# Performance work log

Hardware: AMD Instinct MI355X
Metric: run time of the kernel (lower is better)

Reference implementation:

```python
import jax, jax.numpy as jnp
import numpy as np

EPS = 1e-8
LRELU_SLOPE = 0.2
ACT_GAIN = float(np.sqrt(2.0))  # def_gain for lrelu
GAIN = 1.0                      # forward default
CLAMP = 256.0


def setup_inputs() -> dict:
    key = jax.random.key(0)
    k1, k2 = jax.random.split(key)
    x = jax.random.normal(k1, (8, 128, 32, 32, 32), dtype=jnp.float32)
    weight = jax.random.normal(k2, (128, 128, 3, 3, 3), dtype=jnp.float32)
    bias = jnp.zeros((128,), dtype=jnp.float32)
    return {"x": x, "weight": weight, "bias": bias}


def _modulated_conv3d(x, weight, styles, padding, demodulate=True):
    # x: [B, Cin, D, H, W], weight: [Cout, Cin, kd, kh, kw], styles: [B, Cin]
    w = weight[None] * styles[:, None, :, None, None, None]  # [B, Cout, Cin, kd, kh, kw]
    if demodulate:
        dcoefs = jax.lax.rsqrt(jnp.sum(jnp.square(w), axis=(2, 3, 4, 5)) + EPS)  # [B, Cout]
        w = w * dcoefs[:, :, None, None, None, None]
    pad = [(padding, padding)] * 3

    def per_sample(xi, wi):
        # xi: [Cin, D, H, W], wi: [Cout, Cin, kd, kh, kw]
        return jax.lax.conv_general_dilated(
            xi[None], wi, window_strides=(1, 1, 1), padding=pad,
            dimension_numbers=("NCDHW", "OIDHW", "NCDHW"))[0]

    return jax.vmap(per_sample)(x, w)  # [B, Cout, D, H, W]


def reference(x, weight, bias):
    padding = weight.shape[-1] // 2
    styles = jnp.ones((x.shape[0], weight.shape[1]), dtype=x.dtype)
    y = _modulated_conv3d(x, weight, styles, padding)
    y = jax.nn.leaky_relu(y + bias[None, :, None, None, None], LRELU_SLOPE)
    # clamp_gain(act, act_gain*gain, 256*gain)
    return jnp.clip(y * (ACT_GAIN * GAIN), -CLAMP * GAIN, CLAMP * GAIN)
```

## Files before the change

kernel.cpp:

```cpp
#include <hip/hip_runtime.h>

typedef short bf16x8 __attribute__((ext_vector_type(8)));
typedef float f32x4  __attribute__((ext_vector_type(4)));
typedef unsigned short u16;

static __device__ __forceinline__ u16 f2bf(float f) {
    unsigned int u = __builtin_bit_cast(unsigned int, f);
    u += 0x7FFFu + ((u >> 16) & 1u);
    return (u16)(u >> 16);
}

static __device__ __forceinline__ void gload_lds16(const void* g, void* l) {
    __builtin_amdgcn_global_load_lds((const __attribute__((address_space(1))) void*)g,
                                     (__attribute__((address_space(3))) void*)l, 16, 0, 0);
}

__global__ __launch_bounds__(256) void prep_w_k(const float* __restrict__ w,
                                                u16* __restrict__ wn) {
    const int co = blockIdx.x;
    const int t  = threadIdx.x;
    const float* wc = w + co * 3456;
    float s = 0.f;
    for (int i = t; i < 3456; i += 256) { float v = wc[i]; s += v * v; }
#pragma unroll
    for (int off = 32; off; off >>= 1) s += __shfl_down(s, off);
    __shared__ float red[4];
    __shared__ float dsh;
    if ((t & 63) == 0) red[t >> 6] = s;
    __syncthreads();
    if (t == 0) dsh = rsqrtf(red[0] + red[1] + red[2] + red[3] + 1e-8f);
    __syncthreads();
    const float d = dsh;
    for (int i = t; i < 3456; i += 256) {
        int ci = i / 27, tap = i - ci * 27;
        float v = wc[i] * d;
        wn[((tap * 4 + (ci >> 5)) * 128 + co) * 32 + (ci & 31)] = f2bf(v);
    }
}

__global__ __launch_bounds__(256) void xpose_k(const float* __restrict__ x,
                                               u16* __restrict__ xt) {
    const int bid = blockIdx.x;
    const int b = bid >> 10, d = (bid >> 5) & 31, h = bid & 31;
    const int t = threadIdx.x;
    const int w = t & 31, cg = t >> 5;
    const int base_dhw = d * 1024 + h * 32 + w;
#pragma unroll
    for (int r = 0; r < 2; ++r) {
        int g = cg + r * 8;
        const float* src = x + ((size_t)(b * 128 + g * 8) << 15) + base_dhw;
        bf16x8 pk;
#pragma unroll
        for (int j = 0; j < 8; ++j) pk[j] = (short)f2bf(src[(size_t)j << 15]);
        *(bf16x8*)&xt[((size_t)((b * 16 + g) << 15) + base_dhw) * 8] = pk;
    }
}

#define KSX 1048576
#define KSW 4096
#define RB  24576
__global__ __launch_bounds__(512, 2) void conv_p4(
    const u16* __restrict__ wsb, const float* __restrict__ bias,
    float* __restrict__ out) {
    __shared__ __align__(16) u16 lds[3 * RB];
    const u16* xt = wsb + 524288;
    const u16* wn = wsb + 512;
    const u16* zp = wsb;

    const int t = threadIdx.x, lane = t & 63, wid = t >> 6;
    const int ll = lane & 15, g = lane >> 4;
    const int mslice = wid >> 1, ncol = wid & 1;

    int wg = ((blockIdx.x & 7) << 7) | (blockIdx.x >> 3);
    const int b = wg >> 7, dt = (wg >> 3) & 15, ht = wg & 7;
    const int d0 = dt * 2, h0 = ht * 4;

    const int pos0 = mslice * 64 + ll;
    const int xro = pos0 * 32 + ((g ^ ((pos0 >> 1) & 3)) * 8);
    const int co0 = ncol * 64 + ll;
    const int wro = 16384 + co0 * 32 + ((g ^ ((co0 >> 1) & 3)) * 8);

    const int posA = wid * 32 + (lane >> 2);
    const int slot = lane & 3;
    const int pdA = posA >> 7, phA = (posA >> 5) & 3, wA = posA & 31;
    const int gA = slot ^ ((posA >> 1) & 3);
    const int wco = wid * 16 + (lane >> 2);
    const u16* wsrc = wn + wco * 32 + ((slot ^ ((wco >> 1) & 3)) * 8);

    f32x4 acc[4][4];
#pragma unroll
    for (int i = 0; i < 4; ++i)
#pragma unroll
        for (int j = 0; j < 4; ++j) acc[i][j] = (f32x4){0.f, 0.f, 0.f, 0.f};

    int od_s = 0, oh_s = 0, ow_s = 0, cc_s = 0;
    const u16* xsA = xt; bool okA = false, okB = false;

#define DO_STAGE(SB, H) { \
    if (cc_s == 0) { \
        int Dx = d0 + pdA - 1 + od_s, Hx = h0 + phA - 1 + oh_s, Wx = wA - 1 + ow_s; \
        bool dh_ = ((unsigned)Dx < 32u) && ((unsigned)Hx < 32u); \
        okA = dh_ && ((unsigned)Wx < 32u); \
        okB = dh_ && (Wx < 16); \
        xsA = xt + (long)((b * 16 + gA) * 32768 + Dx * 1024 + Hx * 32 + Wx) * 8; } \
    gload_lds16(okA ? (const void*)xsA : (const void*)zp, \
                (void*)&lds[(SB)*RB + (H)*8192 + wid*1024]); \
    gload_lds16(okB ? (const void*)(xsA + 128) : (const void*)zp, \
                (void*)&lds[(SB)*RB + (H)*8192 + wid*1024 + 512]); \
    gload_lds16((const void*)wsrc, \
                (void*)&lds[(SB)*RB + 16384 + (H)*4096 + wid*512]); \
    xsA += KSX; wsrc += KSW; \
    if (++cc_s == 4) { cc_s = 0; \
        if (++ow_s == 3) { ow_s = 0; if (++oh_s == 3) { oh_s = 0; ++od_s; } } } }

#define MFMA8(P, XP) { \
    __builtin_amdgcn_s_setprio(1); \
    _Pragma("unroll") for (int nf = 0; nf < 4; ++nf) { \
        acc[P][nf] = __builtin_amdgcn_mfma_f32_16x16x32_bf16(wf[nf][0], XP[0], acc[P][nf], 0, 0, 0); \
        acc[P][nf] = __builtin_amdgcn_mfma_f32_16x16x32_bf16(wf[nf][1], XP[1], acc[P][nf], 0, 0, 0); } \
    __builtin_amdgcn_s_setprio(0); }

#define PH_SYNC() { \
    asm volatile("s_waitcnt lgkmcnt(0)" ::: "memory"); \
    asm volatile("s_barrier" ::: "memory"); }

#define ITER(C, S, DOST, VM3) { \
    bf16x8 wf[4][2], x0[2], x1[2], x2[2], x3[2]; \
    _Pragma("unroll") for (int nf = 0; nf < 4; ++nf) { \
        wf[nf][0] = *(const bf16x8*)&lds[(C)*RB + wro + nf * 512]; \
        wf[nf][1] = *(const bf16x8*)&lds[(C)*RB + 4096 + wro + nf * 512]; } \
    x0[0] = *(const bf16x8*)&lds[(C)*RB + xro]; \
    x0[1] = *(const bf16x8*)&lds[(C)*RB + 8192 + xro]; \
    if (DOST) DO_STAGE(S, 0); \
    PH_SYNC(); \
    MFMA8(0, x0); \
    x1[0] = *(const bf16x8*)&lds[(C)*RB + xro + 512]; \
    x1[1] = *(const bf16x8*)&lds[(C)*RB + 8192 + xro + 512]; \
    if (DOST) DO_STAGE(S, 1); \
    PH_SYNC(); \
    MFMA8(1, x1); \
    x2[0] = *(const bf16x8*)&lds[(C)*RB + xro + 1024]; \
    x2[1] = *(const bf16x8*)&lds[(C)*RB + 8192 + xro + 1024]; \
    PH_SYNC(); \
    MFMA8(2, x2); \
    x3[0] = *(const bf16x8*)&lds[(C)*RB + xro + 1536]; \
    x3[1] = *(const bf16x8*)&lds[(C)*RB + 8192 + xro + 1536]; \
    asm volatile("s_waitcnt lgkmcnt(0)" ::: "memory"); \
    asm volatile("s_waitcnt " VM3 ::: "memory"); \
    asm volatile("s_barrier" ::: "memory"); \
    MFMA8(3, x3); }

    DO_STAGE(0, 0); DO_STAGE(0, 1); DO_STAGE(1, 0); DO_STAGE(1, 1);
    asm volatile("s_waitcnt vmcnt(6)" ::: "memory");
    asm volatile("s_barrier" ::: "memory");

    for (int m = 0; m < 17; ++m) {
        ITER(0, 2, 1, "vmcnt(6)");
        ITER(1, 0, 1, "vmcnt(6)");
        ITER(2, 1, 1, "vmcnt(6)");
    }
    ITER(0, 2, 1, "vmcnt(6)");
    ITER(1, 0, 0, "vmcnt(0)");
    ITER(2, 0, 0, "vmcnt(0)");

    const int pd = mslice >> 1, phb = (mslice & 1) * 2;
#pragma unroll
    for (int nf = 0; nf < 4; ++nf) {
        f32x4 bb = *(const f32x4*)&bias[ncol * 64 + nf * 16 + g * 4];
#pragma unroll
        for (int mf = 0; mf < 4; ++mf) {
            const int wq = (mf & 1) * 16 + ll;
            const int hh = h0 + phb + (mf >> 1);
            float* orow = out + ((size_t)(b * 128 + ncol * 64 + nf * 16 + g * 4) << 15)
                          + (d0 + pd) * 1024 + hh * 32 + wq;
#pragma unroll
            for (int q = 0; q < 4; ++q) {
                float v = acc[mf][nf][q] + bb[q];
                v = v > 0.f ? v : v * 0.2f;
                v *= 1.41421356237f;
                v = fminf(fmaxf(v, -256.f), 256.f);
                orow[(size_t)q << 15] = v;
            }
        }
    }
#undef DO_STAGE
#undef MFMA8
#undef PH_SYNC
#undef ITER
}

#define NPOS 544
__global__ __launch_bounds__(256, 4) void conv_fb(
    const float* __restrict__ x, const u16* __restrict__ wn,
    const float* __restrict__ bias, float* __restrict__ out) {
    __shared__ __align__(16) u16 lds[NPOS * 32];
    float* ldsf = reinterpret_cast<float*>(lds);
    const int t = threadIdx.x;
    const int lane = t & 63;
    const int wid  = t >> 6;
    const int wr   = wid >> 1;
    const int wcn  = wid & 1;
    const int ll   = lane & 15;
    const int g    = lane >> 4;
    const int bid = blockIdx.x;
    const int b  = bid >> 8;
    const int dt = (bid >> 4) & 15, ht = bid & 15;
    const int d0 = dt * 2, h0 = ht * 2;
    const int sw  = t & 31;
    const int sg  = (t >> 5) & 3;
    const int rhi = t >> 7;
    f32x4 acc[4][4];
#pragma unroll
    for (int i = 0; i < 4; ++i)
#pragma unroll
        for (int j = 0; j < 4; ++j) acc[i][j] = (f32x4){0.f, 0.f, 0.f, 0.f};
    float bv[4][4];
#pragma unroll
    for (int nf = 0; nf < 4; ++nf) {
        f32x4 bb = *(const f32x4*)&bias[wcn * 64 + nf * 16 + g * 4];
#pragma unroll
        for (int q = 0; q < 4; ++q) bv[nf][q] = bb[q];
    }
    if (t < 128) {
        int pi  = t >> 2;
        int row = pi >> 1;
        int pos = row * 34 + (pi & 1) * 33;
        bf16x8 z = {0, 0, 0, 0, 0, 0, 0, 0};
        *(bf16x8*)&lds[pos * 32 + (t & 3) * 8] = z;
    }
    for (int c = 0; c < 4; ++c) {
        if (c) __syncthreads();
#pragma unroll
        for (int p = 0; p < 8; ++p) {
            int rowid = p * 2 + rhi;
            int pd = rowid >> 2, ph = rowid & 3;
            int d = d0 - 1 + pd, h = h0 - 1 + ph;
            bool ok = ((unsigned)d < 32u) && ((unsigned)h < 32u);
            const float* src = x + (((b * 128 + c * 32 + sg * 8) * 32 + d) * 32 + h) * 32 + sw;
            float v[8];
#pragma unroll
            for (int j = 0; j < 8; ++j) v[j] = ok ? src[j * 32768] : 0.f;
            bf16x8 pk;
#pragma unroll
            for (int j = 0; j < 8; ++j) pk[j] = (short)f2bf(v[j]);
            int pos = rowid * 34 + sw + 1;
            int sl = sg ^ ((pos >> 1) & 3);
            *(bf16x8*)&lds[pos * 32 + sl * 8] = pk;
        }
        __syncthreads();
        const u16* wbase = wn + c * 4096 + ((wcn * 64 + ll) * 32 + g * 8);
        bf16x8 wf[4];
#pragma unroll
        for (int nf = 0; nf < 4; ++nf) wf[nf] = *(const bf16x8*)&wbase[nf * 512];
#pragma unroll
        for (int tap = 0; tap < 27; ++tap) {
            const int od = tap / 9, oh = (tap / 3) % 3, ow = tap % 3;
            bf16x8 wfn[4];
            if (tap < 26) {
#pragma unroll
                for (int nf = 0; nf < 4; ++nf)
                    wfn[nf] = *(const bf16x8*)&wbase[(tap + 1) * 16384 + nf * 512];
            }
            bf16x8 xf[4];
#pragma unroll
            for (int mf = 0; mf < 4; ++mf) {
                int pos = ((wr + od) * 4 + (mf >> 1) + oh) * 34 + (mf & 1) * 16 + ll + ow;
                int sl = g ^ ((pos >> 1) & 3);
                xf[mf] = *(const bf16x8*)&lds[pos * 32 + sl * 8];
            }
            __builtin_amdgcn_s_setprio(1);
#pragma unroll
            for (int mf = 0; mf < 4; ++mf)
#pragma unroll
                for (int nf = 0; nf < 4; ++nf)
                    acc[mf][nf] = __builtin_amdgcn_mfma_f32_16x16x32_bf16(
                        wf[nf], xf[mf], acc[mf][nf], 0, 0, 0);
            __builtin_amdgcn_s_setprio(0);
            if (tap < 26) {
#pragma unroll
                for (int nf = 0; nf < 4; ++nf) wf[nf] = wfn[nf];
            }
        }
    }
#pragma unroll
    for (int p = 0; p < 4; ++p) {
        const int dd = p >> 1, hh = p & 1;
        __syncthreads();
        if (wr == dd) {
#pragma unroll
            for (int whalf = 0; whalf < 2; ++whalf) {
                const int mf = hh * 2 + whalf;
#pragma unroll
                for (int nf = 0; nf < 4; ++nf) {
#pragma unroll
                    for (int q = 0; q < 4; ++q) {
                        const int co = wcn * 64 + nf * 16 + g * 4 + q;
                        float v = acc[mf][nf][q] + bv[nf][q];
                        v = v > 0.f ? v : v * 0.2f;
                        v *= 1.41421356237f;
                        v = fminf(fmaxf(v, -256.f), 256.f);
                        ldsf[co * 33 + whalf * 16 + ll] = v;
                    }
                }
            }
        }
        __syncthreads();
#pragma unroll
        for (int it = 0; it < 4; ++it) {
            const int row = it * 32 + (t >> 3);
            const int ls  = t & 7;
            f32x4 v = *(f32x4*)&ldsf[row * 33 + ls * 4];
            *(f32x4*)&out[(size_t)(b * 128 + row) * 32768 +
                          (d0 + dd) * 1024 + (h0 + hh) * 32 + ls * 4] = v;
        }
    }
}

extern "C" void kernel_launch(void* const* d_in, const int* in_sizes, int n_in,
                              void* d_out, int out_size, void* d_ws, size_t ws_size,
                              hipStream_t stream) {
    const float* x    = (const float*)d_in[0];
    const float* w    = (const float*)d_in[1];
    const float* bias = (const float*)d_in[2];
    float* out        = (float*)d_out;
    u16* wsb          = (u16*)d_ws;

    hipMemsetAsync(d_ws, 0, 1024, stream);
    prep_w_k<<<128, 256, 0, stream>>>(w, wsb + 512);

    if (ws_size >= 68157440ull) {
        xpose_k<<<8192, 256, 0, stream>>>(x, wsb + 524288);
        conv_p4<<<1024, 512, 0, stream>>>(wsb, bias, out);
    } else {
        conv_fb<<<2048, 256, 0, stream>>>(x, wsb + 512, bias, out);
    }
}
```

Measured before the change: 294.7 us.

## Restructure conv main loop to prefetch next stage fragments and loop over weight columns

```diff
diff --git a/kernel.cpp b/kernel.cpp
--- a/kernel.cpp
+++ b/kernel.cpp
@@ -59,7 +59,7 @@
 #define KSX 1048576
 #define KSW 4096
 #define RB  24576
-__global__ __launch_bounds__(512, 2) void conv_p4(
+__global__ __launch_bounds__(512, 2) void conv_m2(
     const u16* __restrict__ wsb, const float* __restrict__ bias,
     float* __restrict__ out) {
     __shared__ __align__(16) u16 lds[3 * RB];
@@ -95,6 +95,9 @@
 
     int od_s = 0, oh_s = 0, ow_s = 0, cc_s = 0;
     const u16* xsA = xt; bool okA = false, okB = false;
+
+    bf16x8 xa[4][2], xb[4][2];
+    bf16x8 wfA[2], wfB[2];
 
 #define DO_STAGE(SB, H) { \
     if (cc_s == 0) { \
@@ -113,55 +116,68 @@
     if (++cc_s == 4) { cc_s = 0; \
         if (++ow_s == 3) { ow_s = 0; if (++oh_s == 3) { oh_s = 0; ++od_s; } } } }
 
-#define MFMA8(P, XP) { \
+#define MFMA8(P, WF, XC) { \
     __builtin_amdgcn_s_setprio(1); \
-    _Pragma("unroll") for (int nf = 0; nf < 4; ++nf) { \
-        acc[P][nf] = __builtin_amdgcn_mfma_f32_16x16x32_bf16(wf[nf][0], XP[0], acc[P][nf], 0, 0, 0); \
-        acc[P][nf] = __builtin_amdgcn_mfma_f32_16x16x32_bf16(wf[nf][1], XP[1], acc[P][nf], 0, 0, 0); } \
+    _Pragma("unroll") for (int mf = 0; mf < 4; ++mf) { \
+        acc[mf][P] = __builtin_amdgcn_mfma_f32_16x16x32_bf16(WF[0], XC[mf][0], acc[mf][P], 0, 0, 0); \
+        acc[mf][P] = __builtin_amdgcn_mfma_f32_16x16x32_bf16(WF[1], XC[mf][1], acc[mf][P], 0, 0, 0); } \
     __builtin_amdgcn_s_setprio(0); }
 
-#define PH_SYNC() { \
+#define BARSYNC() { \
+    asm volatile("s_barrier" ::: "memory"); \
     asm volatile("s_waitcnt lgkmcnt(0)" ::: "memory"); \
-    asm volatile("s_barrier" ::: "memory"); }
-
-#define ITER(C, S, DOST, VM3) { \
-    bf16x8 wf[4][2], x0[2], x1[2], x2[2], x3[2]; \
-    _Pragma("unroll") for (int nf = 0; nf < 4; ++nf) { \
-        wf[nf][0] = *(const bf16x8*)&lds[(C)*RB + wro + nf * 512]; \
-        wf[nf][1] = *(const bf16x8*)&lds[(C)*RB + 4096 + wro + nf * 512]; } \
-    x0[0] = *(const bf16x8*)&lds[(C)*RB + xro]; \
-    x0[1] = *(const bf16x8*)&lds[(C)*RB + 8192 + xro]; \
+    __builtin_amdgcn_sched_barrier(0); }
+#define TBAR() asm volatile("s_barrier" ::: "memory");
+
+#define ITER(C, N, S, XC, XN, DOST, VM, DONEXT) { \
+    wfB[0] = *(const bf16x8*)&lds[(C)*RB + wro + 512]; \
+    wfB[1] = *(const bf16x8*)&lds[(C)*RB + wro + 512 + 4096]; \
     if (DOST) DO_STAGE(S, 0); \
-    PH_SYNC(); \
-    MFMA8(0, x0); \
-    x1[0] = *(const bf16x8*)&lds[(C)*RB + xro + 512]; \
-    x1[1] = *(const bf16x8*)&lds[(C)*RB + 8192 + xro + 512]; \
+    BARSYNC(); MFMA8(0, wfA, XC); TBAR(); \
+    wfA[0] = *(const bf16x8*)&lds[(C)*RB + wro + 1024]; \
+    wfA[1] = *(const bf16x8*)&lds[(C)*RB + wro + 1024 + 4096]; \
     if (DOST) DO_STAGE(S, 1); \
-    PH_SYNC(); \
-    MFMA8(1, x1); \
-    x2[0] = *(const bf16x8*)&lds[(C)*RB + xro + 1024]; \
-    x2[1] = *(const bf16x8*)&lds[(C)*RB + 8192 + xro + 1024]; \
-    PH_SYNC(); \
-    MFMA8(2, x2); \
-    x3[0] = *(const bf16x8*)&lds[(C)*RB + xro + 1536]; \
-    x3[1] = *(const bf16x8*)&lds[(C)*RB + 8192 + xro + 1536]; \
-    asm volatile("s_waitcnt lgkmcnt(0)" ::: "memory"); \
-    asm volatile("s_waitcnt " VM3 ::: "memory"); \
-    asm volatile("s_barrier" ::: "memory"); \
-    MFMA8(3, x3); }
+    BARSYNC(); MFMA8(1, wfB, XC); TBAR(); \
+    wfB[0] = *(const bf16x8*)&lds[(C)*RB + wro + 1536]; \
+    wfB[1] = *(const bf16x8*)&lds[(C)*RB + wro + 1536 + 4096]; \
+    BARSYNC(); MFMA8(2, wfA, XC); \
+    asm volatile("s_waitcnt " VM ::: "memory"); TBAR(); \
+    if (DONEXT) { \
+        _Pragma("unroll") for (int mf = 0; mf < 4; ++mf) { \
+            XN[mf][0] = *(const bf16x8*)&lds[(N)*RB + xro + mf * 512]; \
+            XN[mf][1] = *(const bf16x8*)&lds[(N)*RB + xro + mf * 512 + 8192]; } \
+        wfA[0] = *(const bf16x8*)&lds[(N)*RB + wro]; \
+        wfA[1] = *(const bf16x8*)&lds[(N)*RB + wro + 4096]; } \
+    BARSYNC(); MFMA8(3, wfB, XC); TBAR(); }
 
     DO_STAGE(0, 0); DO_STAGE(0, 1); DO_STAGE(1, 0); DO_STAGE(1, 1);
     asm volatile("s_waitcnt vmcnt(6)" ::: "memory");
     asm volatile("s_barrier" ::: "memory");
-
-    for (int m = 0; m < 17; ++m) {
-        ITER(0, 2, 1, "vmcnt(6)");
-        ITER(1, 0, 1, "vmcnt(6)");
-        ITER(2, 1, 1, "vmcnt(6)");
-    }
-    ITER(0, 2, 1, "vmcnt(6)");
-    ITER(1, 0, 0, "vmcnt(0)");
-    ITER(2, 0, 0, "vmcnt(0)");
+#pragma unroll
+    for (int mf = 0; mf < 4; ++mf) {
+        xa[mf][0] = *(const bf16x8*)&lds[xro + mf * 512];
+        xa[mf][1] = *(const bf16x8*)&lds[xro + mf * 512 + 8192];
+    }
+    wfA[0] = *(const bf16x8*)&lds[wro];
+    wfA[1] = *(const bf16x8*)&lds[wro + 4096];
+    asm volatile("s_waitcnt lgkmcnt(0)" ::: "memory");
+    __builtin_amdgcn_sched_barrier(0);
+    asm volatile("s_barrier" ::: "memory");
+
+    for (int m = 0; m < 8; ++m) {
+        ITER(0, 1, 2, xa, xb, 1, "vmcnt(6)", 1);
+        ITER(1, 2, 0, xb, xa, 1, "vmcnt(6)", 1);
+        ITER(2, 0, 1, xa, xb, 1, "vmcnt(6)", 1);
+        ITER(0, 1, 2, xb, xa, 1, "vmcnt(6)", 1);
+        ITER(1, 2, 0, xa, xb, 1, "vmcnt(6)", 1);
+        ITER(2, 0, 1, xb, xa, 1, "vmcnt(6)", 1);
+    }
+    ITER(0, 1, 2, xa, xb, 1, "vmcnt(6)", 1);
+    ITER(1, 2, 0, xb, xa, 1, "vmcnt(6)", 1);
+    ITER(2, 0, 1, xa, xb, 1, "vmcnt(6)", 1);
+    ITER(0, 1, 2, xb, xa, 1, "vmcnt(6)", 1);
+    ITER(1, 2, 0, xa, xb, 0, "vmcnt(0)", 1);
+    ITER(2, 0, 1, xb, xa, 0, "vmcnt(0)", 0);
 
     const int pd = mslice >> 1, phb = (mslice & 1) * 2;
 #pragma unroll
@@ -185,7 +201,8 @@
     }
 #undef DO_STAGE
 #undef MFMA8
-#undef PH_SYNC
+#undef BARSYNC
+#undef TBAR
 #undef ITER
 }
 
@@ -330,7 +347,7 @@
 
     if (ws_size >= 68157440ull) {
         xpose_k<<<8192, 256, 0, stream>>>(x, wsb + 524288);
-        conv_p4<<<1024, 512, 0, stream>>>(wsb, bias, out);
+        conv_m2<<<1024, 512, 0, stream>>>(wsb, bias, out);
     } else {
         conv_fb<<<2048, 256, 0, stream>>>(x, wsb + 512, bias, out);
     }
```

After: 304.2 us. +3.2%, slower.
